# Performance work log

Measured on AMD Instinct MI355X. Metric: run time of the kernel, lower is better.

The kernel has to match this reference:

```python
import jax, jax.numpy as jnp
import numpy as np

L, H, N = 4096, 256, 64  # seq_len, hidden_size, hippo_n
EPS = 1e-5


def setup_inputs() -> dict:
    key = jax.random.key(0)
    ks = jax.random.split(key, 8)
    x = jax.random.normal(ks[0], (L, H), jnp.float32)
    # S4D-Lin style initialization for the diagonal SSM (H independent SSMs of state size N)
    Lambda_re = -0.5 * jnp.ones((H, N), jnp.float32)
    Lambda_im = jnp.tile(jnp.pi * jnp.arange(N, dtype=jnp.float32), (H, 1))
    B_re = jnp.ones((H, N), jnp.float32)
    B_im = jnp.zeros((H, N), jnp.float32)
    C_re = jax.random.normal(ks[1], (H, N), jnp.float32) * (0.5 ** 0.5)
    C_im = jax.random.normal(ks[2], (H, N), jnp.float32) * (0.5 ** 0.5)
    D = jax.random.normal(ks[3], (H,), jnp.float32)
    log_step = jax.random.uniform(ks[4], (H,), jnp.float32,
                                  minval=jnp.log(0.001), maxval=jnp.log(0.1))
    ln_w = jnp.ones((H,), jnp.float32)
    ln_b = jnp.zeros((H,), jnp.float32)
    sc = 1.0 / jnp.sqrt(jnp.float32(H))
    W1 = jax.random.normal(ks[5], (H, H), jnp.float32) * sc
    b1 = jnp.zeros((H,), jnp.float32)
    W2 = jax.random.normal(ks[6], (H, H), jnp.float32) * sc
    b2 = jnp.zeros((H,), jnp.float32)
    return {"x": x, "Lambda_re": Lambda_re, "Lambda_im": Lambda_im,
            "B_re": B_re, "B_im": B_im, "C_re": C_re, "C_im": C_im,
            "D": D, "log_step": log_step, "ln_w": ln_w, "ln_b": ln_b,
            "W1": W1, "b1": b1, "W2": W2, "b2": b2}


def reference(x, Lambda_re, Lambda_im, B_re, B_im, C_re, C_im, D, log_step,
              ln_w, ln_b, W1, b1, W2, b2):
    skip = x
    # per-token LayerNorm over the H feature axis (eqx.nn.LayerNorm, eps=1e-5)
    mu = jnp.mean(x, axis=-1, keepdims=True)
    var = jnp.mean(jnp.square(x - mu), axis=-1, keepdims=True)
    xn = (x - mu) / jnp.sqrt(var + EPS) * ln_w + ln_b  # [L, H]

    # ZOH discretization of the diagonal SSM (the cell.ssm(L) step)
    Lam = Lambda_re + 1j * Lambda_im                     # [H, N] complex64
    dt = jnp.exp(log_step)[:, None]                      # [H, 1]
    Ab = jnp.exp(Lam * dt)                               # [H, N]
    Bb = (Ab - 1.0) / Lam * (B_re + 1j * B_im)           # [H, N]
    C = C_re + 1j * C_im                                 # [H, N]

    def step(s, u):  # s: [H, N] complex state, u: [H] input at one time step
        s = Ab * s + Bb * u[:, None]
        y = 2.0 * jnp.einsum('hn,hn->h', C, s).real + D * u
        return s, y

    s0 = jnp.zeros((H, N), jnp.complex64)
    hidden, ys = jax.lax.scan(step, s0, xn)              # ys: [L, H]

    g = jax.nn.gelu(ys)
    out = (g @ W1.T + b1) * jax.nn.sigmoid(g @ W2.T + b2)  # GLU epilogue
    return (hidden, skip + out)
```

## Files before the change

kernel.cpp:

```cpp
#include <hip/hip_runtime.h>
#include <hip/hip_bf16.h>

#define LSEQ 4096
#define HDIM 256
#define NS   64
#define PC   32
#define MC   128

typedef __attribute__((ext_vector_type(8))) short short8;
typedef __attribute__((ext_vector_type(4))) float floatx4;

__device__ __forceinline__ float lane_bcast(float v, int j) {
    return __uint_as_float(__builtin_amdgcn_readlane(__float_as_uint(v), j));
}

__global__ __launch_bounds__(256) void k_ln_stats(const float* __restrict__ x,
                                                  float* __restrict__ mu,
                                                  float* __restrict__ rstd,
                                                  const float* __restrict__ W1,
                                                  const float* __restrict__ W2,
                                                  unsigned short* __restrict__ w1b,
                                                  unsigned short* __restrict__ w2b) {
    int t = threadIdx.x;
    if (blockIdx.x >= LSEQ) {
        int g = (blockIdx.x - LSEQ) * 256 + t;
        float4 a = ((const float4*)W1)[g];
        float4 c = ((const float4*)W2)[g];
        ushort4 o1, o2;
        __hip_bfloat16 h;
        h = __float2bfloat16(a.x); o1.x = *(unsigned short*)&h;
        h = __float2bfloat16(a.y); o1.y = *(unsigned short*)&h;
        h = __float2bfloat16(a.z); o1.z = *(unsigned short*)&h;
        h = __float2bfloat16(a.w); o1.w = *(unsigned short*)&h;
        h = __float2bfloat16(c.x); o2.x = *(unsigned short*)&h;
        h = __float2bfloat16(c.y); o2.y = *(unsigned short*)&h;
        h = __float2bfloat16(c.z); o2.z = *(unsigned short*)&h;
        h = __float2bfloat16(c.w); o2.w = *(unsigned short*)&h;
        ((ushort4*)w1b)[g] = o1;
        ((ushort4*)w2b)[g] = o2;
        return;
    }
    int l = blockIdx.x;
    float v = x[l * HDIM + t];
    float s = v, s2 = v * v;
#pragma unroll
    for (int o = 32; o; o >>= 1) {
        s  += __shfl_xor(s, o);
        s2 += __shfl_xor(s2, o);
    }
    __shared__ float ps[4], ps2[4];
    int w = t >> 6;
    if ((t & 63) == 0) { ps[w] = s; ps2[w] = s2; }
    __syncthreads();
    if (t == 0) {
        float S = ps[0] + ps[1] + ps[2] + ps[3];
        float S2 = ps2[0] + ps2[1] + ps2[2] + ps2[3];
        float m = S * (1.0f / HDIM);
        float var = S2 * (1.0f / HDIM) - m * m;
        mu[l] = m;
        rstd[l] = rsqrtf(var + 1e-5f);
    }
}

__global__ __launch_bounds__(256) void k_transnorm(const float* __restrict__ x,
                                                   const float* __restrict__ mu,
                                                   const float* __restrict__ rstd,
                                                   const float* __restrict__ w,
                                                   const float* __restrict__ b,
                                                   float* __restrict__ xnT) {
    __shared__ float tile[64 * 65];
    int l0 = blockIdx.x * 64, h0 = blockIdx.y * 64;
    int t = threadIdx.x;
#pragma unroll
    for (int i = 0; i < 16; ++i) {
        int e = i * 256 + t;
        int r = e >> 6, c = e & 63;
        int l = l0 + r, h = h0 + c;
        float v = x[l * HDIM + h];
        v = (v - mu[l]) * rstd[l] * w[h] + b[h];
        tile[c * 65 + r] = v;
    }
    __syncthreads();
#pragma unroll
    for (int i = 0; i < 16; ++i) {
        int e = i * 256 + t;
        int hh = e >> 6, ll = e & 63;
        xnT[(size_t)(h0 + hh) * LSEQ + l0 + ll] = tile[hh * 65 + ll];
    }
}

__device__ inline void ssm_consts(const float* Lre, const float* Lim,
                                  const float* Bre, const float* Bim,
                                  const float* lstep, int h, int n,
                                  float& are, float& aim, float& bre, float& bim) {
    int idx = h * NS + n;
    float lre = Lre[idx], lim = Lim[idx];
    float dt = expf(lstep[h]);
    float er = expf(lre * dt);
    float sa, ca;
    sincosf(lim * dt, &sa, &ca);
    are = er * ca; aim = er * sa;
    float inv = 1.0f / (lre * lre + lim * lim);
    float nre = are - 1.0f, nim = aim;
    float tre = (nre * lre + nim * lim) * inv;
    float tim = (nim * lre - nre * lim) * inv;
    float br = Bre[idx], bi = Bim[idx];
    bre = tre * br - tim * bi;
    bim = tre * bi + tim * br;
}

__global__ __launch_bounds__(256) void k_scan_local(const float* __restrict__ xnT,
                                                    const float* __restrict__ Lre,
                                                    const float* __restrict__ Lim,
                                                    const float* __restrict__ Bre,
                                                    const float* __restrict__ Bim,
                                                    const float* __restrict__ lstep,
                                                    float2* __restrict__ f) {
    int wv = __builtin_amdgcn_readfirstlane((int)threadIdx.x) >> 6;
    int n = threadIdx.x & 63;
    int c = blockIdx.x * 4 + wv, h = blockIdx.y;
    const float* u = xnT + (size_t)h * LSEQ + c * MC;
    float are, aim, bre, bim;
    ssm_consts(Lre, Lim, Bre, Bim, lstep, h, n, are, aim, bre, bim);
    float sre = 0.f, sim = 0.f;
    for (int g = 0; g < 2; ++g) {
        float uv = u[g * 64 + n];
#pragma unroll
        for (int j = 0; j < 64; ++j) {
            float us = lane_bcast(uv, j);
            float nr = fmaf(are, sre, fmaf(-aim, sim, bre * us));
            float ni = fmaf(are, sim, fmaf( aim, sre, bim * us));
            sre = nr; sim = ni;
        }
    }
    f[(size_t)(h * PC + c) * NS + n] = make_float2(sre, sim);
}

__global__ __launch_bounds__(256) void k_scan_out(const float* __restrict__ xnT,
                                                  const float* __restrict__ Lre,
                                                  const float* __restrict__ Lim,
                                                  const float* __restrict__ Bre,
                                                  const float* __restrict__ Bim,
                                                  const float* __restrict__ Cre,
                                                  const float* __restrict__ Cim,
                                                  const float* __restrict__ Dv,
                                                  const float* __restrict__ lstep,
                                                  const float2* __restrict__ f,
                                                  __hip_bfloat16* __restrict__ gb,
                                                  float* __restrict__ hid,
                                                  int interleaved) {
    __shared__ __align__(16) float red[4][16 * 68];
    int wv = __builtin_amdgcn_readfirstlane((int)threadIdx.x) >> 6;
    int lane = threadIdx.x & 63;
    int c = blockIdx.x * 4 + wv, h = blockIdx.y, n = lane;
    const float* u = xnT + (size_t)h * LSEQ + c * MC;
    float are, aim, bre, bim;
    ssm_consts(Lre, Lim, Bre, Bim, lstep, h, n, are, aim, bre, bim);
    int idx = h * NS + n;
    float cre = Cre[idx], cim = Cim[idx];
    float Dh = Dv[h];

    float ar = are, ai = aim;
#pragma unroll
    for (int q = 0; q < 7; ++q) {
        float r2 = ar * ar - ai * ai;
        ai = 2.f * ar * ai;
        ar = r2;
    }
    float sre = 0.f, sim = 0.f;
    for (int cp = 0; cp < c; ++cp) {
        float2 fc = f[(size_t)(h * PC + cp) * NS + n];
        float nr = fmaf(ar, sre, fmaf(-ai, sim, fc.x));
        float ni = fmaf(ar, sim, fmaf( ai, sre, fc.y));
        sre = nr; sim = ni;
    }

    float* rw = red[wv];
    int t16 = lane & 15, p = lane >> 4;

    for (int g = 0; g < 2; ++g) {
        float uv = u[g * 64 + lane];
#pragma unroll
        for (int jg = 0; jg < 4; ++jg) {
#pragma unroll
            for (int tt = 0; tt < 16; ++tt) {
                float us = lane_bcast(uv, jg * 16 + tt);
                float nr = fmaf(are, sre, fmaf(-aim, sim, bre * us));
                float ni = fmaf(are, sim, fmaf( aim, sre, bim * us));
                sre = nr; sim = ni;
                rw[tt * 68 + n] = fmaf(cre, sre, -(cim * sim));
            }
            float a0 = 0.f;
            const float4* rp = (const float4*)(rw + t16 * 68 + p * 16);
#pragma unroll
            for (int qq = 0; qq < 4; ++qq) {
                float4 v = rp[qq];
                a0 += (v.x + v.y) + (v.z + v.w);
            }
            a0 += __shfl_xor(a0, 16);
            a0 += __shfl_xor(a0, 32);
            float u_tok = __shfl(uv, jg * 16 + t16);
            if (lane < 16) {
                int l = c * MC + g * 64 + jg * 16 + t16;
                float y = fmaf(2.f, a0, Dh * u_tok);
                float z = 0.7978845608028654f * fmaf(0.044715f, y * y * y, y);
                float e = __expf(2.f * z);
                float th = 1.f - 2.f / (e + 1.f);
                float gg = 0.5f * y * (1.f + th);
                gb[(size_t)l * HDIM + h] = __float2bfloat16(gg);
            }
        }
    }

    if (c == PC - 1) {
        if (interleaved) {
            ((float2*)hid)[idx] = make_float2(sre, sim);
        } else {
            hid[idx] = sre;
        }
    }
}

__global__ __launch_bounds__(64) void k_glu_mfma(const unsigned short* __restrict__ gbs,
                                                 const unsigned short* __restrict__ w1b,
                                                 const unsigned short* __restrict__ w2b,
                                                 const float* __restrict__ b1v,
                                                 const float* __restrict__ b2v,
                                                 const float* __restrict__ x,
                                                 float* __restrict__ out) {
    int bx = blockIdx.x;
    int m0 = (bx >> 3) * 32;
    int n0 = (bx & 7) * 32;
    int lane = threadIdx.x;
    int t = lane & 15, q = lane >> 4;

    floatx4 acc[2][2][2];
#pragma unroll
    for (int a = 0; a < 2; ++a)
#pragma unroll
        for (int b = 0; b < 2; ++b)
#pragma unroll
            for (int g = 0; g < 2; ++g)
                acc[a][b][g] = (floatx4){0.f, 0.f, 0.f, 0.f};

    const unsigned short* A0  = gbs + (size_t)(m0 + t) * HDIM + q * 8;
    const unsigned short* A1  = A0 + 16 * HDIM;
    const unsigned short* B10 = w1b + (size_t)(n0 + t) * HDIM + q * 8;
    const unsigned short* B11 = B10 + 16 * HDIM;
    const unsigned short* B20 = w2b + (size_t)(n0 + t) * HDIM + q * 8;
    const unsigned short* B21 = B20 + 16 * HDIM;

#pragma unroll
    for (int ks = 0; ks < 8; ++ks) {
        int off = ks * 32;
        short8 a0  = *(const short8*)(A0  + off);
        short8 a1  = *(const short8*)(A1  + off);
        short8 b10 = *(const short8*)(B10 + off);
        short8 b11 = *(const short8*)(B11 + off);
        short8 b20 = *(const short8*)(B20 + off);
        short8 b21 = *(const short8*)(B21 + off);
        acc[0][0][0] = __builtin_amdgcn_mfma_f32_16x16x32_bf16(a0, b10, acc[0][0][0], 0, 0, 0);
        acc[0][1][0] = __builtin_amdgcn_mfma_f32_16x16x32_bf16(a0, b11, acc[0][1][0], 0, 0, 0);
        acc[1][0][0] = __builtin_amdgcn_mfma_f32_16x16x32_bf16(a1, b10, acc[1][0][0], 0, 0, 0);
        acc[1][1][0] = __builtin_amdgcn_mfma_f32_16x16x32_bf16(a1, b11, acc[1][1][0], 0, 0, 0);
        acc[0][0][1] = __builtin_amdgcn_mfma_f32_16x16x32_bf16(a0, b20, acc[0][0][1], 0, 0, 0);
        acc[0][1][1] = __builtin_amdgcn_mfma_f32_16x16x32_bf16(a0, b21, acc[0][1][1], 0, 0, 0);
        acc[1][0][1] = __builtin_amdgcn_mfma_f32_16x16x32_bf16(a1, b20, acc[1][0][1], 0, 0, 0);
        acc[1][1][1] = __builtin_amdgcn_mfma_f32_16x16x32_bf16(a1, b21, acc[1][1][1], 0, 0, 0);
    }

#pragma unroll
    for (int nt = 0; nt < 2; ++nt) {
        int hh = n0 + nt * 16 + t;
        float bb1 = b1v[hh], bb2 = b2v[hh];
#pragma unroll
        for (int mt = 0; mt < 2; ++mt) {
#pragma unroll
            for (int reg = 0; reg < 4; ++reg) {
                int l = m0 + mt * 16 + q * 4 + reg;
                float a  = acc[mt][nt][0][reg] + bb1;
                float sg = 1.f / (1.f + __expf(-(acc[mt][nt][1][reg] + bb2)));
                out[(size_t)l * HDIM + hh] = fmaf(a, sg, x[(size_t)l * HDIM + hh]);
            }
        }
    }
}

extern "C" void kernel_launch(void* const* d_in, const int* in_sizes, int n_in,
                              void* d_out, int out_size, void* d_ws, size_t ws_size,
                              hipStream_t stream) {
    (void)in_sizes; (void)n_in; (void)ws_size;
    const float* x     = (const float*)d_in[0];
    const float* Lre   = (const float*)d_in[1];
    const float* Lim   = (const float*)d_in[2];
    const float* Bre   = (const float*)d_in[3];
    const float* Bim   = (const float*)d_in[4];
    const float* Cre   = (const float*)d_in[5];
    const float* Cim   = (const float*)d_in[6];
    const float* Dv    = (const float*)d_in[7];
    const float* lstep = (const float*)d_in[8];
    const float* lnw   = (const float*)d_in[9];
    const float* lnb   = (const float*)d_in[10];
    const float* W1    = (const float*)d_in[11];
    const float* b1    = (const float*)d_in[12];
    const float* W2    = (const float*)d_in[13];
    const float* b2    = (const float*)d_in[14];

    float* ws   = (float*)d_ws;
    float* mu   = ws;
    float* rstd = ws + LSEQ;
    float* xnT  = ws + 2 * LSEQ;
    float2* f   = (float2*)(xnT + (size_t)HDIM * LSEQ);
    unsigned short* gb  = (unsigned short*)(f + (size_t)HDIM * PC * NS);
    unsigned short* w1b = gb + (size_t)LSEQ * HDIM;
    unsigned short* w2b = w1b + HDIM * HDIM;

    int interleaved = (out_size == LSEQ * HDIM + 2 * HDIM * NS) ? 1 : 0;
    float* hid  = (float*)d_out;
    float* outp = (float*)d_out + (interleaved ? 2 * HDIM * NS : HDIM * NS);

    k_ln_stats   <<<LSEQ + 64, 256, 0, stream>>>(x, mu, rstd, W1, W2, w1b, w2b);
    k_transnorm  <<<dim3(LSEQ / 64, HDIM / 64), 256, 0, stream>>>(x, mu, rstd, lnw, lnb, xnT);
    k_scan_local <<<dim3(PC / 4, HDIM), 256, 0, stream>>>(xnT, Lre, Lim, Bre, Bim, lstep, f);
    k_scan_out   <<<dim3(PC / 4, HDIM), 256, 0, stream>>>(xnT, Lre, Lim, Bre, Bim, Cre, Cim,
                                                          Dv, lstep, f, (__hip_bfloat16*)gb,
                                                          hid, interleaved);
    k_glu_mfma   <<<128 * 8, 64, 0, stream>>>(gb, w1b, w2b, b1, b2, x, outp);
}
```

Baseline: 139.0 us.

## Fuse LN stats with transpose-normalize and merge chunked scan into one kernel

Merges LayerNorm statistics and the normalize-transpose into a single kernel that stages 16 tokens in shared memory and writes xnT with float4 stores. Combines the local chunk scan, the cross-chunk carry propagation and the output pass into one 1024-thread block per hidden channel. Chunk carries now pass through shared memory instead of a global buffer, and the prefix loop is done once by one wave rather than redundantly in every chunk's wave. This removes two kernel launches and the global round trips for mu/rstd and chunk states. In exchange it runs only 256 large blocks for the scan and adds block-wide synchronisation, and the output reduction group shrinks from 16 to 8 tokens.

```diff
diff --git a/kernel.cpp b/kernel.cpp
--- a/kernel.cpp
+++ b/kernel.cpp
@@ -14,79 +14,71 @@
     return __uint_as_float(__builtin_amdgcn_readlane(__float_as_uint(v), j));
 }
 
-__global__ __launch_bounds__(256) void k_ln_stats(const float* __restrict__ x,
-                                                  float* __restrict__ mu,
-                                                  float* __restrict__ rstd,
-                                                  const float* __restrict__ W1,
-                                                  const float* __restrict__ W2,
-                                                  unsigned short* __restrict__ w1b,
-                                                  unsigned short* __restrict__ w2b) {
+__global__ __launch_bounds__(256) void k_pre(const float* __restrict__ x,
+                                             const float* __restrict__ lnw,
+                                             const float* __restrict__ lnb,
+                                             const float* __restrict__ W1,
+                                             const float* __restrict__ W2,
+                                             float* __restrict__ xnT,
+                                             unsigned short* __restrict__ w1b,
+                                             unsigned short* __restrict__ w2b) {
     int t = threadIdx.x;
-    if (blockIdx.x >= LSEQ) {
-        int g = (blockIdx.x - LSEQ) * 256 + t;
+    if (blockIdx.x >= 256) {
+        int g = (blockIdx.x - 256) * 256 + t;
         float4 a = ((const float4*)W1)[g];
         float4 c = ((const float4*)W2)[g];
         ushort4 o1, o2;
-        __hip_bfloat16 h;
-        h = __float2bfloat16(a.x); o1.x = *(unsigned short*)&h;
-        h = __float2bfloat16(a.y); o1.y = *(unsigned short*)&h;
-        h = __float2bfloat16(a.z); o1.z = *(unsigned short*)&h;
-        h = __float2bfloat16(a.w); o1.w = *(unsigned short*)&h;
-        h = __float2bfloat16(c.x); o2.x = *(unsigned short*)&h;
-        h = __float2bfloat16(c.y); o2.y = *(unsigned short*)&h;
-        h = __float2bfloat16(c.z); o2.z = *(unsigned short*)&h;
-        h = __float2bfloat16(c.w); o2.w = *(unsigned short*)&h;
+        __hip_bfloat16 hh;
+        hh = __float2bfloat16(a.x); o1.x = *(unsigned short*)&hh;
+        hh = __float2bfloat16(a.y); o1.y = *(unsigned short*)&hh;
+        hh = __float2bfloat16(a.z); o1.z = *(unsigned short*)&hh;
+        hh = __float2bfloat16(a.w); o1.w = *(unsigned short*)&hh;
+        hh = __float2bfloat16(c.x); o2.x = *(unsigned short*)&hh;
+        hh = __float2bfloat16(c.y); o2.y = *(unsigned short*)&hh;
+        hh = __float2bfloat16(c.z); o2.z = *(unsigned short*)&hh;
+        hh = __float2bfloat16(c.w); o2.w = *(unsigned short*)&hh;
         ((ushort4*)w1b)[g] = o1;
         ((ushort4*)w2b)[g] = o2;
         return;
     }
-    int l = blockIdx.x;
-    float v = x[l * HDIM + t];
-    float s = v, s2 = v * v;
-#pragma unroll
-    for (int o = 32; o; o >>= 1) {
-        s  += __shfl_xor(s, o);
-        s2 += __shfl_xor(s2, o);
-    }
-    __shared__ float ps[4], ps2[4];
-    int w = t >> 6;
-    if ((t & 63) == 0) { ps[w] = s; ps2[w] = s2; }
+    __shared__ float tile[16][257];
+    __shared__ float smu[16], srs[16];
+    int l0 = blockIdx.x * 16;
+#pragma unroll
+    for (int i = 0; i < 16; ++i)
+        tile[i][t] = x[(size_t)(l0 + i) * HDIM + t];
     __syncthreads();
-    if (t == 0) {
-        float S = ps[0] + ps[1] + ps[2] + ps[3];
-        float S2 = ps2[0] + ps2[1] + ps2[2] + ps2[3];
-        float m = S * (1.0f / HDIM);
-        float var = S2 * (1.0f / HDIM) - m * m;
-        mu[l] = m;
-        rstd[l] = rsqrtf(var + 1e-5f);
-    }
-}
-
-__global__ __launch_bounds__(256) void k_transnorm(const float* __restrict__ x,
-                                                   const float* __restrict__ mu,
-                                                   const float* __restrict__ rstd,
-                                                   const float* __restrict__ w,
-                                                   const float* __restrict__ b,
-                                                   float* __restrict__ xnT) {
-    __shared__ float tile[64 * 65];
-    int l0 = blockIdx.x * 64, h0 = blockIdx.y * 64;
-    int t = threadIdx.x;
-#pragma unroll
-    for (int i = 0; i < 16; ++i) {
-        int e = i * 256 + t;
-        int r = e >> 6, c = e & 63;
-        int l = l0 + r, h = h0 + c;
-        float v = x[l * HDIM + h];
-        v = (v - mu[l]) * rstd[l] * w[h] + b[h];
-        tile[c * 65 + r] = v;
+    int wv = t >> 6, lane = t & 63;
+#pragma unroll
+    for (int k = 0; k < 4; ++k) {
+        int i = wv * 4 + k;
+        float s = 0.f, s2 = 0.f;
+#pragma unroll
+        for (int q = 0; q < 4; ++q) {
+            float v = tile[i][lane + 64 * q];
+            s += v; s2 += v * v;
+        }
+#pragma unroll
+        for (int o = 32; o; o >>= 1) {
+            s  += __shfl_xor(s, o);
+            s2 += __shfl_xor(s2, o);
+        }
+        if (lane == 0) {
+            float m = s * (1.0f / HDIM);
+            smu[i] = m;
+            srs[i] = rsqrtf(s2 * (1.0f / HDIM) - m * m + 1e-5f);
+        }
     }
     __syncthreads();
-#pragma unroll
-    for (int i = 0; i < 16; ++i) {
-        int e = i * 256 + t;
-        int hh = e >> 6, ll = e & 63;
-        xnT[(size_t)(h0 + hh) * LSEQ + l0 + ll] = tile[hh * 65 + ll];
-    }
+    float wh = lnw[t], bh = lnb[t];
+    float o[16];
+#pragma unroll
+    for (int i = 0; i < 16; ++i)
+        o[i] = (tile[i][t] - smu[i]) * srs[i] * wh + bh;
+    float4* dst = (float4*)(xnT + (size_t)t * LSEQ + l0);
+#pragma unroll
+    for (int k = 0; k < 4; ++k)
+        dst[k] = make_float4(o[4 * k], o[4 * k + 1], o[4 * k + 2], o[4 * k + 3]);
 }
 
 __device__ inline void ssm_consts(const float* Lre, const float* Lim,
@@ -109,114 +101,112 @@
     bim = tre * bi + tim * br;
 }
 
-__global__ __launch_bounds__(256) void k_scan_local(const float* __restrict__ xnT,
-                                                    const float* __restrict__ Lre,
-                                                    const float* __restrict__ Lim,
-                                                    const float* __restrict__ Bre,
-                                                    const float* __restrict__ Bim,
-                                                    const float* __restrict__ lstep,
-                                                    float2* __restrict__ f) {
+__global__ __launch_bounds__(1024) void k_scan(const float* __restrict__ xnT,
+                                               const float* __restrict__ Lre,
+                                               const float* __restrict__ Lim,
+                                               const float* __restrict__ Bre,
+                                               const float* __restrict__ Bim,
+                                               const float* __restrict__ Cre,
+                                               const float* __restrict__ Cim,
+                                               const float* __restrict__ Dv,
+                                               const float* __restrict__ lstep,
+                                               __hip_bfloat16* __restrict__ gb,
+                                               float* __restrict__ hid,
+                                               int interleaved) {
+    __shared__ float2 fst[PC * NS];
+    __shared__ __align__(16) float red[16][8 * 68];
+    int h = blockIdx.x;
     int wv = __builtin_amdgcn_readfirstlane((int)threadIdx.x) >> 6;
-    int n = threadIdx.x & 63;
-    int c = blockIdx.x * 4 + wv, h = blockIdx.y;
-    const float* u = xnT + (size_t)h * LSEQ + c * MC;
-    float are, aim, bre, bim;
-    ssm_consts(Lre, Lim, Bre, Bim, lstep, h, n, are, aim, bre, bim);
-    float sre = 0.f, sim = 0.f;
-    for (int g = 0; g < 2; ++g) {
-        float uv = u[g * 64 + n];
-#pragma unroll
-        for (int j = 0; j < 64; ++j) {
-            float us = lane_bcast(uv, j);
-            float nr = fmaf(are, sre, fmaf(-aim, sim, bre * us));
-            float ni = fmaf(are, sim, fmaf( aim, sre, bim * us));
-            sre = nr; sim = ni;
-        }
-    }
-    f[(size_t)(h * PC + c) * NS + n] = make_float2(sre, sim);
-}
-
-__global__ __launch_bounds__(256) void k_scan_out(const float* __restrict__ xnT,
-                                                  const float* __restrict__ Lre,
-                                                  const float* __restrict__ Lim,
-                                                  const float* __restrict__ Bre,
-                                                  const float* __restrict__ Bim,
-                                                  const float* __restrict__ Cre,
-                                                  const float* __restrict__ Cim,
-                                                  const float* __restrict__ Dv,
-                                                  const float* __restrict__ lstep,
-                                                  const float2* __restrict__ f,
-                                                  __hip_bfloat16* __restrict__ gb,
-                                                  float* __restrict__ hid,
-                                                  int interleaved) {
-    __shared__ __align__(16) float red[4][16 * 68];
-    int wv = __builtin_amdgcn_readfirstlane((int)threadIdx.x) >> 6;
-    int lane = threadIdx.x & 63;
-    int c = blockIdx.x * 4 + wv, h = blockIdx.y, n = lane;
-    const float* u = xnT + (size_t)h * LSEQ + c * MC;
+    int lane = threadIdx.x & 63, n = lane;
+    const float* uh = xnT + (size_t)h * LSEQ;
+
     float are, aim, bre, bim;
     ssm_consts(Lre, Lim, Bre, Bim, lstep, h, n, are, aim, bre, bim);
     int idx = h * NS + n;
     float cre = Cre[idx], cim = Cim[idx];
     float Dh = Dv[h];
 
-    float ar = are, ai = aim;
-#pragma unroll
-    for (int q = 0; q < 7; ++q) {
-        float r2 = ar * ar - ai * ai;
-        ai = 2.f * ar * ai;
-        ar = r2;
-    }
-    float sre = 0.f, sim = 0.f;
-    for (int cp = 0; cp < c; ++cp) {
-        float2 fc = f[(size_t)(h * PC + cp) * NS + n];
-        float nr = fmaf(ar, sre, fmaf(-ai, sim, fc.x));
-        float ni = fmaf(ar, sim, fmaf( ai, sre, fc.y));
-        sre = nr; sim = ni;
-    }
-
-    float* rw = red[wv];
-    int t16 = lane & 15, p = lane >> 4;
-
-    for (int g = 0; g < 2; ++g) {
-        float uv = u[g * 64 + lane];
-#pragma unroll
-        for (int jg = 0; jg < 4; ++jg) {
-#pragma unroll
-            for (int tt = 0; tt < 16; ++tt) {
-                float us = lane_bcast(uv, jg * 16 + tt);
+#pragma unroll
+    for (int cc = 0; cc < 2; ++cc) {
+        int c = wv * 2 + cc;
+        const float* u = uh + c * MC;
+        float sre = 0.f, sim = 0.f;
+        for (int g = 0; g < 2; ++g) {
+            float uv = u[g * 64 + lane];
+#pragma unroll
+            for (int j = 0; j < 64; ++j) {
+                float us = lane_bcast(uv, j);
                 float nr = fmaf(are, sre, fmaf(-aim, sim, bre * us));
                 float ni = fmaf(are, sim, fmaf( aim, sre, bim * us));
                 sre = nr; sim = ni;
-                rw[tt * 68 + n] = fmaf(cre, sre, -(cim * sim));
             }
-            float a0 = 0.f;
-            const float4* rp = (const float4*)(rw + t16 * 68 + p * 16);
-#pragma unroll
-            for (int qq = 0; qq < 4; ++qq) {
-                float4 v = rp[qq];
-                a0 += (v.x + v.y) + (v.z + v.w);
-            }
-            a0 += __shfl_xor(a0, 16);
-            a0 += __shfl_xor(a0, 32);
-            float u_tok = __shfl(uv, jg * 16 + t16);
-            if (lane < 16) {
-                int l = c * MC + g * 64 + jg * 16 + t16;
-                float y = fmaf(2.f, a0, Dh * u_tok);
-                float z = 0.7978845608028654f * fmaf(0.044715f, y * y * y, y);
-                float e = __expf(2.f * z);
-                float th = 1.f - 2.f / (e + 1.f);
-                float gg = 0.5f * y * (1.f + th);
-                gb[(size_t)l * HDIM + h] = __float2bfloat16(gg);
-            }
-        }
-    }
-
-    if (c == PC - 1) {
+        }
+        fst[c * NS + n] = make_float2(sre, sim);
+    }
+    __syncthreads();
+
+    if (wv == 0) {
+        float ar = are, ai = aim;
+#pragma unroll
+        for (int q = 0; q < 7; ++q) {
+            float r2 = ar * ar - ai * ai;
+            ai = 2.f * ar * ai;
+            ar = r2;
+        }
+        float sre = 0.f, sim = 0.f;
+        for (int c = 0; c < PC; ++c) {
+            float2 fc = fst[c * NS + n];
+            fst[c * NS + n] = make_float2(sre, sim);
+            float nr = fmaf(ar, sre, fmaf(-ai, sim, fc.x));
+            float ni = fmaf(ar, sim, fmaf( ai, sre, fc.y));
+            sre = nr; sim = ni;
+        }
         if (interleaved) {
             ((float2*)hid)[idx] = make_float2(sre, sim);
         } else {
             hid[idx] = sre;
+        }
+    }
+    __syncthreads();
+
+    float* rw = red[wv];
+    int t8 = lane & 7, p = lane >> 3;
+#pragma unroll
+    for (int cc = 0; cc < 2; ++cc) {
+        int c = wv * 2 + cc;
+        const float* u = uh + c * MC;
+        float2 s00 = fst[c * NS + n];
+        float sre = s00.x, sim = s00.y;
+        for (int g = 0; g < 2; ++g) {
+            float uv = u[g * 64 + lane];
+#pragma unroll
+            for (int jg = 0; jg < 8; ++jg) {
+#pragma unroll
+                for (int tt = 0; tt < 8; ++tt) {
+                    float us = lane_bcast(uv, jg * 8 + tt);
+                    float nr = fmaf(are, sre, fmaf(-aim, sim, bre * us));
+                    float ni = fmaf(are, sim, fmaf( aim, sre, bim * us));
+                    sre = nr; sim = ni;
+                    rw[tt * 68 + n] = fmaf(cre, sre, -(cim * sim));
+                }
+                const float4* rp = (const float4*)(rw + t8 * 68 + p * 8);
+                float4 v0 = rp[0], v1 = rp[1];
+                float a0 = ((v0.x + v0.y) + (v0.z + v0.w)) +
+                           ((v1.x + v1.y) + (v1.z + v1.w));
+                a0 += __shfl_xor(a0, 8);
+                a0 += __shfl_xor(a0, 16);
+                a0 += __shfl_xor(a0, 32);
+                float u_tok = __shfl(uv, jg * 8 + t8);
+                if (lane < 8) {
+                    int l = c * MC + g * 64 + jg * 8 + t8;
+                    float y = fmaf(2.f, a0, Dh * u_tok);
+                    float z = 0.7978845608028654f * fmaf(0.044715f, y * y * y, y);
+                    float e = __expf(2.f * z);
+                    float th = 1.f - 2.f / (e + 1.f);
+                    float gg = 0.5f * y * (1.f + th);
+                    gb[(size_t)l * HDIM + h] = __float2bfloat16(gg);
+                }
+            }
         }
     }
 }
@@ -307,11 +297,8 @@
     const float* b2    = (const float*)d_in[14];
 
     float* ws   = (float*)d_ws;
-    float* mu   = ws;
-    float* rstd = ws + LSEQ;
-    float* xnT  = ws + 2 * LSEQ;
-    float2* f   = (float2*)(xnT + (size_t)HDIM * LSEQ);
-    unsigned short* gb  = (unsigned short*)(f + (size_t)HDIM * PC * NS);
+    float* xnT  = ws;
+    unsigned short* gb  = (unsigned short*)(xnT + (size_t)HDIM * LSEQ);
     unsigned short* w1b = gb + (size_t)LSEQ * HDIM;
     unsigned short* w2b = w1b + HDIM * HDIM;
 
@@ -319,11 +306,8 @@
     float* hid  = (float*)d_out;
     float* outp = (float*)d_out + (interleaved ? 2 * HDIM * NS : HDIM * NS);
 
-    k_ln_stats   <<<LSEQ + 64, 256, 0, stream>>>(x, mu, rstd, W1, W2, w1b, w2b);
-    k_transnorm  <<<dim3(LSEQ / 64, HDIM / 64), 256, 0, stream>>>(x, mu, rstd, lnw, lnb, xnT);
-    k_scan_local <<<dim3(PC / 4, HDIM), 256, 0, stream>>>(xnT, Lre, Lim, Bre, Bim, lstep, f);
-    k_scan_out   <<<dim3(PC / 4, HDIM), 256, 0, stream>>>(xnT, Lre, Lim, Bre, Bim, Cre, Cim,
-                                                          Dv, lstep, f, (__hip_bfloat16*)gb,
-                                                          hid, interleaved);
-    k_glu_mfma   <<<128 * 8, 64, 0, stream>>>(gb, w1b, w2b, b1, b2, x, outp);
-}
+    k_pre      <<<256 + 64, 256, 0, stream>>>(x, lnw, lnb, W1, W2, xnT, w1b, w2b);
+    k_scan     <<<HDIM, 1024, 0, stream>>>(xnT, Lre, Lim, Bre, Bim, Cre, Cim,
+                                           Dv, lstep, (__hip_bfloat16*)gb, hid, interleaved);
+    k_glu_mfma <<<128 * 8, 64, 0, stream>>>(gb, w1b, w2b, b1, b2, x, outp);
+}
```

After: 135.9 us. -2.2%, faster.
